# Optimization experiments

Measured on AMD Instinct MI355X. Metric: run time of the kernel, lower is better.

Reference implementation:

```python
import jax, jax.numpy as jnp
import numpy as np

B, S, D, H = 2, 2048, 1024, 16
DK = D // H  # 64


def rotate_half(x):
    d = x.shape[-1]
    x1, x2 = x[..., : d // 2], x[..., d // 2 :]
    return jnp.concatenate([-x2, x1], axis=-1)


def apply_rope(q, k):
    # q, k: [B, H, S, DK]
    d_k = q.shape[-1]
    seq_len = q.shape[-2]
    theta = 10000.0 ** (-2.0 / d_k * jnp.arange(d_k // 2, dtype=q.dtype))
    positions = jnp.arange(seq_len, dtype=q.dtype)
    angles = jnp.outer(positions, theta)                    # [S, DK/2]
    cos = jnp.tile(jnp.cos(angles), (1, 2))                 # [S, DK]
    sin = jnp.tile(jnp.sin(angles), (1, 2))
    q = q * cos + rotate_half(q) * sin
    k = k * cos + rotate_half(k) * sin
    return q, k


def setup_inputs() -> dict:
    key = jax.random.key(0)
    ks = jax.random.split(key, 9)
    std = 1.0 / np.sqrt(D)
    x = jax.random.normal(ks[0], (B, S, D), dtype=jnp.float32)
    # mask True = masked (code uses masked_fill(mask, -inf)); causal mask
    mask = jnp.triu(jnp.ones((S, S), dtype=bool), k=1)[None, None, :, :]
    mask = jnp.broadcast_to(mask, (B, 1, S, S))
    Wq = jax.random.uniform(ks[1], (D, D), jnp.float32, -std, std)
    bq = jax.random.uniform(ks[2], (D,), jnp.float32, -std, std)
    Wk = jax.random.uniform(ks[3], (D, D), jnp.float32, -std, std)
    bk = jax.random.uniform(ks[4], (D,), jnp.float32, -std, std)
    Wv = jax.random.uniform(ks[5], (D, D), jnp.float32, -std, std)
    bv = jax.random.uniform(ks[6], (D,), jnp.float32, -std, std)
    Wo = jax.random.uniform(ks[7], (D, D), jnp.float32, -std, std)
    bo = jax.random.uniform(ks[8], (D,), jnp.float32, -std, std)
    return {"x": x, "mask": mask, "Wq": Wq, "bq": bq, "Wk": Wk, "bk": bk,
            "Wv": Wv, "bv": bv, "Wo": Wo, "bo": bo}


def reference(x, mask, Wq, bq, Wk, bk, Wv, bv, Wo, bo):
    b, s, d = x.shape
    # projections -> [B, H, S, DK]
    q = (x @ Wq + bq).reshape(b, s, H, DK).transpose(0, 2, 1, 3)
    k = (x @ Wk + bk).reshape(b, s, H, DK).transpose(0, 2, 1, 3)
    v = (x @ Wv + bv).reshape(b, s, H, DK).transpose(0, 2, 1, 3)
    q, k = apply_rope(q, k)
    scores = jnp.einsum("bhqd,bhkd->bhqk", q, k) / np.sqrt(DK)
    scores = jnp.where(mask, -jnp.inf, scores)
    probs = jax.nn.softmax(scores, axis=-1)
    attn = jnp.einsum("bhqk,bhkd->bhqd", probs, v)
    o = attn.transpose(0, 2, 1, 3).reshape(b, s, H * DK)
    return o @ Wo + bo
```

## Files before the change

kernel.cpp:

```cpp
#include <hip/hip_runtime.h>
#include <hip/hip_bf16.h>
#include <math.h>

typedef __hip_bfloat16 bf16;
typedef __attribute__((ext_vector_type(8))) short short8;
typedef __attribute__((ext_vector_type(4))) short s16x4;
typedef __attribute__((ext_vector_type(4))) float f32x4;

#define B_  2
#define S_  2048
#define D_  1024
#define H_  16
#define DK_ 64

#define QSCALE 0.18033688011112043f
#define EXPOFF 11.541560327111707f

__device__ inline short bfs(float f) { return __builtin_bit_cast(short, __float2bfloat16(f)); }

#define GLL16(gptr, lptr)                                                        \
    __builtin_amdgcn_global_load_lds(                                            \
        (const __attribute__((address_space(1))) void*)(gptr),                   \
        (__attribute__((address_space(3))) void*)(lptr), 16, 0, 0)

#if __has_builtin(__builtin_amdgcn_mfma_f32_16x16x16bf16_1k)
#define MFMA_16x16x16(A, Bv, C) __builtin_amdgcn_mfma_f32_16x16x16bf16_1k(A, Bv, C, 0, 0, 0)
#elif __has_builtin(__builtin_amdgcn_mfma_f32_16x16x16_bf16)
#define MFMA_16x16x16(A, Bv, C) __builtin_amdgcn_mfma_f32_16x16x16_bf16(A, Bv, C, 0, 0, 0)
#else
static __device__ inline f32x4 mfma16_asm(s16x4 a, s16x4 b, f32x4 c) {
    f32x4 d;
    asm volatile("v_mfma_f32_16x16x16_bf16 %0, %1, %2, %3\n\ts_nop 7\n\ts_nop 7"
                 : "=v"(d) : "v"(a), "v"(b), "v"(c));
    return d;
}
#define MFMA_16x16x16(A, Bv, C) mfma16_asm(A, Bv, C)
#endif

__global__ __launch_bounds__(256)
void prep_k(const float* __restrict__ x,
            const float* __restrict__ W0, const float* __restrict__ W1,
            const float* __restrict__ W2, const float* __restrict__ W3,
            bf16* __restrict__ cx, bf16* __restrict__ Wt)
{
    const int z = blockIdx.z;
    const int t = threadIdx.x;
    if (z == 4) {
        const int bid = blockIdx.y * 16 + blockIdx.x;
        #pragma unroll
        for (int i = 0; i < 16; i++) {
            const size_t g = ((size_t)bid * 256 + t) * 4 + (size_t)i * 262144;
            const float4 v = *(const float4*)(x + g);
            s16x4 o = { bfs(v.x), bfs(v.y), bfs(v.z), bfs(v.w) };
            *(s16x4*)(cx + g) = o;
        }
        return;
    }
    __shared__ float Lt[64][65];
    const float* W = (z == 0) ? W0 : (z == 1) ? W1 : (z == 2) ? W2 : W3;
    bf16* dst = Wt + (size_t)z * D_ * D_;
    const int k0 = blockIdx.y * 64, n0 = blockIdx.x * 64;
    #pragma unroll
    for (int p = 0; p < 4; p++) {
        const int idx = p * 256 + t;
        const int row = idx >> 4, cb = (idx & 15) * 4;
        const float4 v = *(const float4*)(W + (size_t)(k0 + row) * D_ + n0 + cb);
        Lt[cb + 0][row] = v.x; Lt[cb + 1][row] = v.y;
        Lt[cb + 2][row] = v.z; Lt[cb + 3][row] = v.w;
    }
    __syncthreads();
    #pragma unroll
    for (int p = 0; p < 4; p++) {
        const int idx = p * 256 + t;
        const int n = idx >> 4, kb = (idx & 15) * 4;
        s16x4 o = { bfs(Lt[n][kb]), bfs(Lt[n][kb + 1]), bfs(Lt[n][kb + 2]), bfs(Lt[n][kb + 3]) };
        *(s16x4*)(dst + (size_t)(n0 + n) * D_ + k0 + kb) = o;
    }
}

template<int MODE>
__global__ __launch_bounds__(256)
void gemm_k(const bf16* __restrict__ A, const bf16* __restrict__ WtAll,
            const float* __restrict__ b0, const float* __restrict__ b1,
            const float* __restrict__ b2,
            bf16* __restrict__ d0, bf16* __restrict__ d1, bf16* __restrict__ d2,
            float* __restrict__ fout)
{
    constexpr int K = D_;
    const int L = (int)blockIdx.x;
    const int m0 = (L & 31) * 128;
    const int rest = L >> 5;
    const int z = (MODE == 0) ? (rest >> 4) : 3;
    const int n0 = (MODE == 0) ? (rest & 15) * 64 : rest * 64;
    const bf16* W = WtAll + (size_t)z * D_ * D_;
    const float* bias = (MODE == 1) ? b0 : ((z == 0) ? b0 : (z == 1) ? b1 : b2);

    __shared__ __align__(16) short As[128 * 32];
    __shared__ __align__(16) short Bs[64 * 32];

    const int t = threadIdx.x;
    const int wave = t >> 6, lane = t & 63, quad = lane >> 4, l16 = lane & 15;
    const int wm = wave * 32;

    const bf16* gA0 = A + (size_t)(m0 + (t >> 2)) * K + (t & 3) * 8;
    const bf16* gA1 = gA0 + (size_t)64 * K;
    const bf16* gW0 = W + (size_t)(n0 + (t >> 2)) * K + (t & 3) * 8;
    const int wb = wave * 512;

    f32x4 acc[2][4] = {};

    for (int k0 = 0; k0 < K; k0 += 32) {
        __syncthreads();
        GLL16(gA0 + k0, &As[wb]);
        GLL16(gA1 + k0, &As[2048 + wb]);
        GLL16(gW0 + k0, &Bs[wb]);
        __syncthreads();
        short8 af[2], bf[4];
        #pragma unroll
        for (int i = 0; i < 2; i++) af[i] = *(const short8*)&As[(wm + i * 16 + l16) * 32 + quad * 8];
        #pragma unroll
        for (int j = 0; j < 4; j++) bf[j] = *(const short8*)&Bs[(j * 16 + l16) * 32 + quad * 8];
        #pragma unroll
        for (int i = 0; i < 2; i++)
            #pragma unroll
            for (int j = 0; j < 4; j++)
                acc[i][j] = __builtin_amdgcn_mfma_f32_16x16x32_bf16(af[i], bf[j], acc[i][j], 0, 0, 0);
    }

    if (MODE == 1) {
        #pragma unroll
        for (int j = 0; j < 4; j++) {
            const int ncol = n0 + j * 16 + l16;
            const float bb = bias[ncol];
            #pragma unroll
            for (int i = 0; i < 2; i++) {
                const int mbase = m0 + wm + i * 16 + quad * 4;
                #pragma unroll
                for (int r = 0; r < 4; r++)
                    fout[(size_t)(mbase + r) * D_ + ncol] = acc[i][j][r] + bb;
            }
        }
    } else if (z == 2) {
        const int h = n0 >> 6;
        #pragma unroll
        for (int j = 0; j < 4; j++) {
            const int ncol = n0 + j * 16 + l16;
            const float bb = bias[ncol];
            const int dk = ncol & 63;
            #pragma unroll
            for (int i = 0; i < 2; i++) {
                const int mbase = m0 + wm + i * 16 + quad * 4;
                #pragma unroll
                for (int r = 0; r < 4; r++) {
                    const int m = mbase + r;
                    const int b = m >> 11, s = m & (S_ - 1);
                    d2[(((size_t)(b * H_ + h)) * DK_ + dk) * S_ + s] = __float2bfloat16(acc[i][j][r] + bb);
                }
            }
        }
    } else {
        bf16* dst = z ? d1 : d0;
        const float sc = z ? 1.0f : QSCALE;
        const int h = n0 >> 6;
        #pragma unroll
        for (int j = 0; j < 2; j++) {
            const int dk = j * 16 + l16;
            const float th = exp2f((float)dk * -0.41524101186092029f);
            const float blo = bias[(h << 6) + dk];
            const float bhi = bias[(h << 6) + dk + 32];
            #pragma unroll
            for (int i = 0; i < 2; i++) {
                #pragma unroll
                for (int r = 0; r < 4; r++) {
                    const int m = m0 + wm + i * 16 + quad * 4 + r;
                    const int b = m >> 11, s = m & (S_ - 1);
                    float sn, cs;
                    sincosf((float)s * th, &sn, &cs);
                    const float v1 = acc[i][j][r] + blo;
                    const float v2 = acc[i][j + 2][r] + bhi;
                    bf16* p = dst + (((size_t)(b * H_ + h)) * S_ + s) * DK_;
                    p[dk]      = __float2bfloat16((v1 * cs - v2 * sn) * sc);
                    p[dk + 32] = __float2bfloat16((v2 * cs + v1 * sn) * sc);
                }
            }
        }
    }
}

__device__ __forceinline__
void attn_tile(const short* __restrict__ Ks, const short* __restrict__ Vts,
               const short8 qf0, const short8 qf1,
               f32x4* ot, float& l_acc,
               const bool diag, const int wave, const int quad, const int l16)
{
    const int kkmax = diag ? wave : 3;
    for (int kk = 0; kk <= kkmax; kk++) {
        const short8 kf0 = *(const short8*)&Ks[(kk * 16 + l16) * 72 + quad * 8];
        const short8 kf1 = *(const short8*)&Ks[(kk * 16 + l16) * 72 + 32 + quad * 8];
        f32x4 st = {};
        st = __builtin_amdgcn_mfma_f32_16x16x32_bf16(kf0, qf0, st, 0, 0, 0);
        st = __builtin_amdgcn_mfma_f32_16x16x32_bf16(kf1, qf1, st, 0, 0, 0);

        s16x4 pt;
        float psum = 0.0f;
        #pragma unroll
        for (int r = 0; r < 4; r++) {
            const bool masked = diag && (kk == wave) && (quad * 4 + r > l16);
            const float p = masked ? 0.0f : exp2f(st[r] - EXPOFF);
            psum += p;
            pt[r] = bfs(p);
        }
        l_acc += psum;

        #pragma unroll
        for (int dt = 0; dt < 4; dt++) {
            const s16x4 vf = *(const s16x4*)&Vts[(dt * 16 + l16) * 72 + kk * 16 + quad * 4];
            ot[dt] = MFMA_16x16x16(vf, pt, ot[dt]);
        }
    }
}

__global__ __launch_bounds__(256)
void attn_k(const bf16* __restrict__ q_ws, const bf16* __restrict__ k_ws,
            const bf16* __restrict__ vt_ws, bf16* __restrict__ attn_ws)
{
    __shared__ __align__(16) short Ks[64 * 72];
    __shared__ __align__(16) short Vts[64 * 72];

    const int linear = (int)blockIdx.y * 16 + (int)blockIdx.x;
    const int bh = linear & 31;
    const int pr = linear >> 5;
    const int qtA = pr, qtB = 31 - pr;
    const int t = threadIdx.x;
    const int wave = t >> 6, quad = (t & 63) >> 4, l16 = t & 15;
    const bf16* Kb = k_ws + (size_t)bh * S_ * DK_;
    const bf16* Vb = vt_ws + (size_t)bh * DK_ * S_;
    const int b = bh >> 4, h = bh & 15;

    const bf16* QbA = q_ws + ((size_t)bh * S_ + qtA * 64 + wave * 16) * DK_;
    const bf16* QbB = q_ws + ((size_t)bh * S_ + qtB * 64 + wave * 16) * DK_;
    const short8 qfA0 = *(const short8*)(QbA + (size_t)l16 * DK_ + quad * 8);
    const short8 qfA1 = *(const short8*)(QbA + (size_t)l16 * DK_ + 32 + quad * 8);
    const short8 qfB0 = *(const short8*)(QbB + (size_t)l16 * DK_ + quad * 8);
    const short8 qfB1 = *(const short8*)(QbB + (size_t)l16 * DK_ + 32 + quad * 8);

    float lA = 0.0f, lB = 0.0f;
    f32x4 otA[4] = {}, otB[4] = {};

    for (int kt = 0; kt <= qtB; kt++) {
        __syncthreads();
        #pragma unroll
        for (int p = 0; p < 2; p++) {
            const int idx = p * 256 + t;
            const int row = idx >> 3, cb = (idx & 7) * 8;
            *(float4*)&Ks[row * 72 + cb]  = *(const float4*)(Kb + (size_t)(kt * 64 + row) * DK_ + cb);
            *(float4*)&Vts[row * 72 + cb] = *(const float4*)(Vb + (size_t)row * S_ + kt * 64 + cb);
        }
        __syncthreads();

        if (kt <= qtA)
            attn_tile(Ks, Vts, qfA0, qfA1, otA, lA, kt == qtA, wave, quad, l16);
        attn_tile(Ks, Vts, qfB0, qfB1, otB, lB, kt == qtB, wave, quad, l16);
    }

    #pragma unroll
    for (int which = 0; which < 2; which++) {
        float l_acc = which ? lB : lA;
        f32x4* ot = which ? otB : otA;
        const int q0 = (which ? qtB : qtA) * 64;
        l_acc += __shfl_xor(l_acc, 16, 64);
        l_acc += __shfl_xor(l_acc, 32, 64);
        const float inv = 1.0f / l_acc;
        const int srow = q0 + wave * 16 + l16;
        bf16* orow = attn_ws + ((size_t)(b * S_ + srow)) * D_ + h * 64;
        #pragma unroll
        for (int dt = 0; dt < 4; dt++) {
            s16x4 o4 = { bfs(ot[dt][0] * inv), bfs(ot[dt][1] * inv),
                         bfs(ot[dt][2] * inv), bfs(ot[dt][3] * inv) };
            *(s16x4*)(orow + dt * 16 + quad * 4) = o4;
        }
    }
}

extern "C" void kernel_launch(void* const* d_in, const int* in_sizes, int n_in,
                              void* d_out, int out_size, void* d_ws, size_t ws_size,
                              hipStream_t stream)
{
    (void)out_size; (void)ws_size;
    const float* x = nullptr;
    const float* W[4] = {nullptr, nullptr, nullptr, nullptr};
    const float* bias[4] = {nullptr, nullptr, nullptr, nullptr};
    int wi = 0, bi = 0;
    for (int i = 0; i < n_in; i++) {
        const int sz = in_sizes[i];
        if (sz == B_ * S_ * D_ && x == nullptr) x = (const float*)d_in[i];
        else if (sz == D_ * D_ && wi < 4) W[wi++] = (const float*)d_in[i];
        else if (sz == D_ && bi < 4) bias[bi++] = (const float*)d_in[i];
    }

    bf16* ws = (bf16*)d_ws;
    const size_t SEG = (size_t)B_ * S_ * D_;
    bf16* canonX  = ws;
    bf16* Wt      = ws + SEG;
    bf16* k_ws    = ws + 2 * SEG;
    bf16* vt_ws   = ws + 3 * SEG;
    bf16* attn_ws = canonX;
    bf16* q_ws    = (bf16*)d_out;

    prep_k<<<dim3(16, 16, 5), 256, 0, stream>>>(x, W[0], W[1], W[2], W[3], canonX, Wt);

    gemm_k<0><<<dim3(1536, 1, 1), 256, 0, stream>>>(
        canonX, Wt, bias[0], bias[1], bias[2], q_ws, k_ws, vt_ws, nullptr);

    attn_k<<<dim3(16, B_ * H_), 256, 0, stream>>>(q_ws, k_ws, vt_ws, attn_ws);

    gemm_k<1><<<dim3(512, 1, 1), 256, 0, stream>>>(
        attn_ws, Wt, bias[3], nullptr, nullptr, nullptr, nullptr, nullptr,
        (float*)d_out);
}
```

Before: 228.6 us.

## Split attention into one query tile per block and shrink output GEMM tile

The attention kernel now launches one block per (head, query tile), 1024 blocks, with heaviest tiles scheduled first. Before, each of 512 blocks handled a pair of complementary query tiles that shared K/V loads. The output projection GEMM is templated on its M tile and now uses 64-row tiles, doubling its block count to 1024. Both changes aim for more parallelism and better fill of the many CUs. The cost is that each K/V tile is loaded from memory twice as often in attention, and the GEMM reuses each B tile less.

Result: slower. 242.1 us (+5.9%).

```diff
diff --git a/kernel.cpp b/kernel.cpp
--- a/kernel.cpp
+++ b/kernel.cpp
@@ -78,7 +78,7 @@
     }
 }
 
-template<int MODE>
+template<int MODE, int TM>
 __global__ __launch_bounds__(256)
 void gemm_k(const bf16* __restrict__ A, const bf16* __restrict__ WtAll,
             const float* __restrict__ b0, const float* __restrict__ b1,
@@ -87,41 +87,43 @@
             float* __restrict__ fout)
 {
     constexpr int K = D_;
+    constexpr int MT = (B_ * S_) / TM;
+    constexpr int AI = TM / 64;
     const int L = (int)blockIdx.x;
-    const int m0 = (L & 31) * 128;
-    const int rest = L >> 5;
+    const int m0 = (L & (MT - 1)) * TM;
+    const int rest = L / MT;
     const int z = (MODE == 0) ? (rest >> 4) : 3;
     const int n0 = (MODE == 0) ? (rest & 15) * 64 : rest * 64;
     const bf16* W = WtAll + (size_t)z * D_ * D_;
     const float* bias = (MODE == 1) ? b0 : ((z == 0) ? b0 : (z == 1) ? b1 : b2);
 
-    __shared__ __align__(16) short As[128 * 32];
+    __shared__ __align__(16) short As[TM * 32];
     __shared__ __align__(16) short Bs[64 * 32];
 
     const int t = threadIdx.x;
     const int wave = t >> 6, lane = t & 63, quad = lane >> 4, l16 = lane & 15;
-    const int wm = wave * 32;
+    const int wm = wave * (TM / 4);
 
     const bf16* gA0 = A + (size_t)(m0 + (t >> 2)) * K + (t & 3) * 8;
     const bf16* gA1 = gA0 + (size_t)64 * K;
     const bf16* gW0 = W + (size_t)(n0 + (t >> 2)) * K + (t & 3) * 8;
     const int wb = wave * 512;
 
-    f32x4 acc[2][4] = {};
+    f32x4 acc[AI][4] = {};
 
     for (int k0 = 0; k0 < K; k0 += 32) {
         __syncthreads();
         GLL16(gA0 + k0, &As[wb]);
-        GLL16(gA1 + k0, &As[2048 + wb]);
+        if (TM == 128) GLL16(gA1 + k0, &As[2048 + wb]);
         GLL16(gW0 + k0, &Bs[wb]);
         __syncthreads();
-        short8 af[2], bf[4];
-        #pragma unroll
-        for (int i = 0; i < 2; i++) af[i] = *(const short8*)&As[(wm + i * 16 + l16) * 32 + quad * 8];
+        short8 af[AI], bf[4];
+        #pragma unroll
+        for (int i = 0; i < AI; i++) af[i] = *(const short8*)&As[(wm + i * 16 + l16) * 32 + quad * 8];
         #pragma unroll
         for (int j = 0; j < 4; j++) bf[j] = *(const short8*)&Bs[(j * 16 + l16) * 32 + quad * 8];
         #pragma unroll
-        for (int i = 0; i < 2; i++)
+        for (int i = 0; i < AI; i++)
             #pragma unroll
             for (int j = 0; j < 4; j++)
                 acc[i][j] = __builtin_amdgcn_mfma_f32_16x16x32_bf16(af[i], bf[j], acc[i][j], 0, 0, 0);
@@ -133,7 +135,7 @@
             const int ncol = n0 + j * 16 + l16;
             const float bb = bias[ncol];
             #pragma unroll
-            for (int i = 0; i < 2; i++) {
+            for (int i = 0; i < AI; i++) {
                 const int mbase = m0 + wm + i * 16 + quad * 4;
                 #pragma unroll
                 for (int r = 0; r < 4; r++)
@@ -148,7 +150,7 @@
             const float bb = bias[ncol];
             const int dk = ncol & 63;
             #pragma unroll
-            for (int i = 0; i < 2; i++) {
+            for (int i = 0; i < AI; i++) {
                 const int mbase = m0 + wm + i * 16 + quad * 4;
                 #pragma unroll
                 for (int r = 0; r < 4; r++) {
@@ -169,7 +171,7 @@
             const float blo = bias[(h << 6) + dk];
             const float bhi = bias[(h << 6) + dk + 32];
             #pragma unroll
-            for (int i = 0; i < 2; i++) {
+            for (int i = 0; i < AI; i++) {
                 #pragma unroll
                 for (int r = 0; r < 4; r++) {
                     const int m = m0 + wm + i * 16 + quad * 4 + r;
@@ -227,27 +229,23 @@
     __shared__ __align__(16) short Ks[64 * 72];
     __shared__ __align__(16) short Vts[64 * 72];
 
-    const int linear = (int)blockIdx.y * 16 + (int)blockIdx.x;
-    const int bh = linear & 31;
-    const int pr = linear >> 5;
-    const int qtA = pr, qtB = 31 - pr;
+    const int bh = (int)blockIdx.x;
+    const int qt = 31 - (int)blockIdx.y;
+    const int q0 = qt * 64;
     const int t = threadIdx.x;
     const int wave = t >> 6, quad = (t & 63) >> 4, l16 = t & 15;
     const bf16* Kb = k_ws + (size_t)bh * S_ * DK_;
     const bf16* Vb = vt_ws + (size_t)bh * DK_ * S_;
     const int b = bh >> 4, h = bh & 15;
 
-    const bf16* QbA = q_ws + ((size_t)bh * S_ + qtA * 64 + wave * 16) * DK_;
-    const bf16* QbB = q_ws + ((size_t)bh * S_ + qtB * 64 + wave * 16) * DK_;
-    const short8 qfA0 = *(const short8*)(QbA + (size_t)l16 * DK_ + quad * 8);
-    const short8 qfA1 = *(const short8*)(QbA + (size_t)l16 * DK_ + 32 + quad * 8);
-    const short8 qfB0 = *(const short8*)(QbB + (size_t)l16 * DK_ + quad * 8);
-    const short8 qfB1 = *(const short8*)(QbB + (size_t)l16 * DK_ + 32 + quad * 8);
-
-    float lA = 0.0f, lB = 0.0f;
-    f32x4 otA[4] = {}, otB[4] = {};
-
-    for (int kt = 0; kt <= qtB; kt++) {
+    const bf16* Qb = q_ws + ((size_t)bh * S_ + q0 + wave * 16) * DK_;
+    const short8 qf0 = *(const short8*)(Qb + (size_t)l16 * DK_ + quad * 8);
+    const short8 qf1 = *(const short8*)(Qb + (size_t)l16 * DK_ + 32 + quad * 8);
+
+    float l_acc = 0.0f;
+    f32x4 ot[4] = {};
+
+    for (int kt = 0; kt <= qt; kt++) {
         __syncthreads();
         #pragma unroll
         for (int p = 0; p < 2; p++) {
@@ -258,27 +256,19 @@
         }
         __syncthreads();
 
-        if (kt <= qtA)
-            attn_tile(Ks, Vts, qfA0, qfA1, otA, lA, kt == qtA, wave, quad, l16);
-        attn_tile(Ks, Vts, qfB0, qfB1, otB, lB, kt == qtB, wave, quad, l16);
-    }
-
+        attn_tile(Ks, Vts, qf0, qf1, ot, l_acc, kt == qt, wave, quad, l16);
+    }
+
+    l_acc += __shfl_xor(l_acc, 16, 64);
+    l_acc += __shfl_xor(l_acc, 32, 64);
+    const float inv = 1.0f / l_acc;
+    const int srow = q0 + wave * 16 + l16;
+    bf16* orow = attn_ws + ((size_t)(b * S_ + srow)) * D_ + h * 64;
     #pragma unroll
-    for (int which = 0; which < 2; which++) {
-        float l_acc = which ? lB : lA;
-        f32x4* ot = which ? otB : otA;
-        const int q0 = (which ? qtB : qtA) * 64;
-        l_acc += __shfl_xor(l_acc, 16, 64);
-        l_acc += __shfl_xor(l_acc, 32, 64);
-        const float inv = 1.0f / l_acc;
-        const int srow = q0 + wave * 16 + l16;
-        bf16* orow = attn_ws + ((size_t)(b * S_ + srow)) * D_ + h * 64;
-        #pragma unroll
-        for (int dt = 0; dt < 4; dt++) {
-            s16x4 o4 = { bfs(ot[dt][0] * inv), bfs(ot[dt][1] * inv),
-                         bfs(ot[dt][2] * inv), bfs(ot[dt][3] * inv) };
-            *(s16x4*)(orow + dt * 16 + quad * 4) = o4;
-        }
+    for (int dt = 0; dt < 4; dt++) {
+        s16x4 o4 = { bfs(ot[dt][0] * inv), bfs(ot[dt][1] * inv),
+                     bfs(ot[dt][2] * inv), bfs(ot[dt][3] * inv) };
+        *(s16x4*)(orow + dt * 16 + quad * 4) = o4;
     }
 }
 
@@ -309,12 +299,12 @@
 
     prep_k<<<dim3(16, 16, 5), 256, 0, stream>>>(x, W[0], W[1], W[2], W[3], canonX, Wt);
 
-    gemm_k<0><<<dim3(1536, 1, 1), 256, 0, stream>>>(
+    gemm_k<0, 128><<<dim3(1536, 1, 1), 256, 0, stream>>>(
         canonX, Wt, bias[0], bias[1], bias[2], q_ws, k_ws, vt_ws, nullptr);
 
-    attn_k<<<dim3(16, B_ * H_), 256, 0, stream>>>(q_ws, k_ws, vt_ws, attn_ws);
-
-    gemm_k<1><<<dim3(512, 1, 1), 256, 0, stream>>>(
+    attn_k<<<dim3(32, 32), 256, 0, stream>>>(q_ws, k_ws, vt_ws, attn_ws);
+
+    gemm_k<1, 64><<<dim3(1024, 1, 1), 256, 0, stream>>>(
         attn_ws, Wt, bias[3], nullptr, nullptr, nullptr, nullptr, nullptr,
         (float*)d_out);
 }
```
